# Kernel tuning notes

Measured on AMD Instinct MI355X. Metric: run time of the kernel, lower is better.

Reference implementation:

```python
import jax, jax.numpy as jnp
import numpy as np

SUBDIVISIONS = 3  # init_kwargs
EPS = 1e-6


def setup_inputs() -> dict:
    key = jax.random.key(0)
    k1, k2, k3 = jax.random.split(key, 3)
    V, K, F = 100000, 32, 64
    features = jax.random.normal(k1, (V, F), dtype=jnp.float32)
    distsq = jax.random.uniform(k2, (V, K), dtype=jnp.float32)
    neighbour_indices = jax.random.randint(k3, (V, K), 0, V, dtype=jnp.int32)
    length_scale = jnp.float32(1.0)  # non-trainable Variable, init 1.0
    return {"features": features, "distsq": distsq,
            "neighbour_indices": neighbour_indices, "length_scale": length_scale}


def reference(features, distsq, neighbour_indices, length_scale):
    # Inference path: no length-scale EMA update (training=None -> in_train_phase takes the
    # unchanged value), distsq is stop-gradient.
    distsq = jax.lax.stop_gradient(distsq)
    scaler = 10.0 * length_scale * float(SUBDIVISIONS)
    d = jnp.sqrt(distsq + EPS)                      # (V, K) neighbor distances
    nfeat = features[neighbour_indices]             # (V, K, F) gathered neighbor features
    outs = []
    for i in range(SUBDIVISIONS):
        offset = float(i) / length_scale            # radius-bin center
        w = jnp.exp(-scaler * (d - offset) ** 2)    # (V, K) Gaussian radius-bin weights
        num = jnp.einsum('vk,vkf->vf', w, nfeat)    # weighted sum over neighbors
        den = jnp.sum(w, axis=1, keepdims=True) + EPS
        outs.append(num / den)                      # soft-pixel weighted mean
    return jnp.concatenate(outs, axis=1)            # (V, SUBDIVISIONS * F)
```

## Files before the change

kernel.cpp:

```cpp
#include <hip/hip_runtime.h>

#define SP_EPS 1e-6f
typedef float f32x2 __attribute__((ext_vector_type(2)));

__device__ __forceinline__ unsigned short bf16_rne(float x) {
    unsigned u = __float_as_uint(x);
    unsigned r = u + 0x7fffu + ((u >> 16) & 1u);
    return (unsigned short)(r >> 16);
}

__global__ __launch_bounds__(256) void f32_to_bf16_kernel(
    const float* __restrict__ in, unsigned short* __restrict__ outb, int n4)
{
    int i = blockIdx.x * 256 + threadIdx.x;
    if (i >= n4) return;
    const float4 v = ((const float4*)in)[i];
    ushort4 o;
    o.x = bf16_rne(v.x); o.y = bf16_rne(v.y);
    o.z = bf16_rne(v.z); o.w = bf16_rne(v.w);
    ((ushort4*)outb)[i] = o;
}

__global__ __launch_bounds__(256) void softpixel_pk_kernel(
    const unsigned short* __restrict__ fb,
    const float* __restrict__ distsq,
    const int*   __restrict__ nidx,
    const float* __restrict__ ls_ptr,
    float*       __restrict__ out,
    int V)
{
    __shared__ f32x2 w01buf[4][32];
    __shared__ f32x2 iw2buf[4][32];
    const int lane = threadIdx.x & 63;
    const int wv   = threadIdx.x >> 6;
    const int v    = blockIdx.x * 4 + wv;
    const int h    = lane >> 5;
    const int j    = lane & 31;
    const int vc   = v < V ? v : V - 1;

    const float ls     = ls_ptr[0];
    const float scaler = 30.0f * ls;
    const float inv_ls = 1.0f / ls;

    const unsigned dvoff = (unsigned)vc * 32u + (unsigned)j;
    const float dsq = distsq[dvoff];
    const int   nb  = nidx[dvoff];
    const float d   = sqrtf(dsq + SP_EPS);
    const float t1  = d - inv_ls;
    const float t2  = d - 2.0f * inv_ls;
    const float w0  = __expf(-scaler * d  * d);
    const float w1  = __expf(-scaler * t1 * t1);
    const float w2  = __expf(-scaler * t2 * t2);
    if (h == 0) {
        w01buf[wv][j] = (f32x2){w0, w1};
        iw2buf[wv][j] = (f32x2){__int_as_float(nb), w2};
    }

    float s0 = w0, s1 = w1, s2 = w2;
    #pragma unroll
    for (int st = 1; st < 32; st <<= 1) {
        s0 += __shfl_xor(s0, st, 64);
        s1 += __shfl_xor(s1, st, 64);
        s2 += __shfl_xor(s2, st, 64);
    }
    s0 += SP_EPS; s1 += SP_EPS; s2 += SP_EPS;
    __syncthreads();

    f32x2 a01_0 = {0.f, 0.f};
    f32x2 a01_1 = {0.f, 0.f};
    float a2_0 = 0.f, a2_1 = 0.f;
    const unsigned j4 = (unsigned)(j << 2);

    #pragma unroll
    for (int kk = 0; kk < 16; ++kk) {
        const f32x2 w01 = w01buf[wv][2 * kk + h];
        const f32x2 iw2 = iw2buf[wv][2 * kk + h];
        const int   ik  = __float_as_int(iw2.x);
        const unsigned boff = ((unsigned)ik << 7) + j4;
        const unsigned fp = *(const unsigned*)((const char*)fb + boff);
        const float f0 = __uint_as_float(fp << 16);
        const float f1 = __uint_as_float(fp & 0xffff0000u);
        f32x2 f01; f01.x = f0; f01.y = f1;
        asm("v_pk_fma_f32 %0, %1, %2, %0 op_sel:[0,0,0] op_sel_hi:[1,0,1]"
            : "+v"(a01_0) : "v"(w01), "v"(f01));
        asm("v_pk_fma_f32 %0, %1, %2, %0 op_sel:[0,1,0] op_sel_hi:[1,1,1]"
            : "+v"(a01_1) : "v"(w01), "v"(f01));
        a2_0 = fmaf(iw2.y, f0, a2_0);
        a2_1 = fmaf(iw2.y, f1, a2_1);
    }

    a01_0.x += __shfl_xor(a01_0.x, 32, 64);
    a01_0.y += __shfl_xor(a01_0.y, 32, 64);
    a01_1.x += __shfl_xor(a01_1.x, 32, 64);
    a01_1.y += __shfl_xor(a01_1.y, 32, 64);
    a2_0 += __shfl_xor(a2_0, 32, 64);
    a2_1 += __shfl_xor(a2_1, 32, 64);

    if (h == 0 && v < V) {
        const float r0 = __builtin_amdgcn_rcpf(s0);
        const float r1 = __builtin_amdgcn_rcpf(s1);
        const float r2 = __builtin_amdgcn_rcpf(s2);
        float* o = out + (unsigned)v * 192u + (unsigned)(j << 1);
        o[0]   = a01_0.x * r0;  o[1]   = a01_1.x * r0;
        o[64]  = a01_0.y * r1;  o[65]  = a01_1.y * r1;
        o[128] = a2_0   * r2;   o[129] = a2_1   * r2;
    }
}

__global__ __launch_bounds__(256) void softpixel_f32_kernel(
    const float* __restrict__ feat,
    const float* __restrict__ distsq,
    const int*   __restrict__ nidx,
    const float* __restrict__ ls_ptr,
    float*       __restrict__ out,
    int V)
{
    const int lane = threadIdx.x & 63;
    const int wv   = threadIdx.x >> 6;
    const int v    = blockIdx.x * 4 + wv;
    if (v >= V) return;

    const float ls     = ls_ptr[0];
    const float scaler = 30.0f * ls;
    const float inv_ls = 1.0f / ls;

    float w0 = 0.f, w1 = 0.f, w2 = 0.f;
    int nb = 0;
    if (lane < 32) {
        const float dsq = distsq[v * 32 + lane];
        nb = nidx[v * 32 + lane];
        const float d  = sqrtf(dsq + SP_EPS);
        const float t1 = d - inv_ls;
        const float t2 = d - 2.0f * inv_ls;
        w0 = __expf(-scaler * d  * d);
        w1 = __expf(-scaler * t1 * t1);
        w2 = __expf(-scaler * t2 * t2);
    }

    float a0 = 0.f, a1 = 0.f, a2 = 0.f;
    float s0 = SP_EPS, s1 = SP_EPS, s2 = SP_EPS;
    #pragma unroll
    for (int k = 0; k < 32; ++k) {
        const int   ik = __shfl(nb, k, 64);
        const float u0 = __shfl(w0, k, 64);
        const float u1 = __shfl(w1, k, 64);
        const float u2 = __shfl(w2, k, 64);
        const float f  = feat[(size_t)ik * 64 + lane];
        a0 = fmaf(u0, f, a0);
        a1 = fmaf(u1, f, a1);
        a2 = fmaf(u2, f, a2);
        s0 += u0; s1 += u1; s2 += u2;
    }
    float* o = out + (size_t)v * 192 + lane;
    o[0]   = a0 / s0;
    o[64]  = a1 / s1;
    o[128] = a2 / s2;
}

extern "C" void kernel_launch(void* const* d_in, const int* in_sizes, int n_in,
                              void* d_out, int out_size, void* d_ws, size_t ws_size,
                              hipStream_t stream) {
    const float* feat   = (const float*)d_in[0];
    const float* distsq = (const float*)d_in[1];
    const int*   nidx   = (const int*)d_in[2];
    const float* ls     = (const float*)d_in[3];

    const int V = in_sizes[1] / 32;
    const int F = in_sizes[0] / V;
    float* out = (float*)d_out;

    const size_t need = (size_t)V * F * sizeof(unsigned short);
    const int grid = (V + 3) / 4;

    if ((size_t)ws_size >= need && F == 64) {
        unsigned short* fb = (unsigned short*)d_ws;
        const int n4 = V * F / 4;
        f32_to_bf16_kernel<<<(n4 + 255) / 256, 256, 0, stream>>>(feat, fb, n4);
        softpixel_pk_kernel<<<grid, 256, 0, stream>>>(fb, distsq, nidx, ls, out, V);
    } else {
        softpixel_f32_kernel<<<grid, 256, 0, stream>>>(feat, distsq, nidx, ls, out, V);
    }
}
```

Before: 72.43 us.

## Switch feature staging to fp16 and use v_fma_mix with permlane32 reduction

Feature rows are now staged as fp16 using packed round-toward-zero conversion instead of a manual bf16 rounding. The main kernel feeds the packed halves straight into v_fma_mix_f32, which removes the unpack shifts and masks. It also merges the per-neighbour LDS data into a single float4 read and replaces the six cross-half shuffles with three v_permlane32_swap instructions plus adds, so every lane now stores one output. Features with large magnitudes could overflow fp16 range, and round-toward-zero adds a small bias.

```diff
diff --git a/kernel.cpp b/kernel.cpp
--- a/kernel.cpp
+++ b/kernel.cpp
@@ -1,27 +1,23 @@
 #include <hip/hip_runtime.h>
 
 #define SP_EPS 1e-6f
-typedef float f32x2 __attribute__((ext_vector_type(2)));
+typedef __fp16 h2 __attribute__((ext_vector_type(2)));
 
-__device__ __forceinline__ unsigned short bf16_rne(float x) {
-    unsigned u = __float_as_uint(x);
-    unsigned r = u + 0x7fffu + ((u >> 16) & 1u);
-    return (unsigned short)(r >> 16);
-}
-
-__global__ __launch_bounds__(256) void f32_to_bf16_kernel(
-    const float* __restrict__ in, unsigned short* __restrict__ outb, int n4)
+__global__ __launch_bounds__(256) void f32_to_f16_kernel(
+    const float* __restrict__ in, unsigned* __restrict__ outh, int n4)
 {
     int i = blockIdx.x * 256 + threadIdx.x;
     if (i >= n4) return;
     const float4 v = ((const float4*)in)[i];
-    ushort4 o;
-    o.x = bf16_rne(v.x); o.y = bf16_rne(v.y);
-    o.z = bf16_rne(v.z); o.w = bf16_rne(v.w);
-    ((ushort4*)outb)[i] = o;
+    h2 p0 = __builtin_amdgcn_cvt_pkrtz(v.x, v.y);
+    h2 p1 = __builtin_amdgcn_cvt_pkrtz(v.z, v.w);
+    uint2 o;
+    o.x = *(unsigned*)&p0;
+    o.y = *(unsigned*)&p1;
+    ((uint2*)outh)[i] = o;
 }
 
-__global__ __launch_bounds__(256) void softpixel_pk_kernel(
+__global__ __launch_bounds__(256) void softpixel_mix_kernel(
     const unsigned short* __restrict__ fb,
     const float* __restrict__ distsq,
     const int*   __restrict__ nidx,
@@ -29,8 +25,7 @@
     float*       __restrict__ out,
     int V)
 {
-    __shared__ f32x2 w01buf[4][32];
-    __shared__ f32x2 iw2buf[4][32];
+    __shared__ float4 qbuf[4][32];
     const int lane = threadIdx.x & 63;
     const int wv   = threadIdx.x >> 6;
     const int v    = blockIdx.x * 4 + wv;
@@ -51,9 +46,31 @@
     const float w0  = __expf(-scaler * d  * d);
     const float w1  = __expf(-scaler * t1 * t1);
     const float w2  = __expf(-scaler * t2 * t2);
-    if (h == 0) {
-        w01buf[wv][j] = (f32x2){w0, w1};
-        iw2buf[wv][j] = (f32x2){__int_as_float(nb), w2};
+    if (h == 0)
+        qbuf[wv][j] = make_float4(__int_as_float(nb), w0, w1, w2);
+    __syncthreads();
+
+    float a0l = 0.f, a0h = 0.f, a1l = 0.f, a1h = 0.f, a2l = 0.f, a2h = 0.f;
+    const unsigned j4 = (unsigned)(j << 2);
+
+    #pragma unroll
+    for (int kk = 0; kk < 16; ++kk) {
+        const float4 q = qbuf[wv][2 * kk + h];
+        const int    ik = __float_as_int(q.x);
+        const unsigned boff = ((unsigned)ik << 7) + j4;
+        const unsigned fp = *(const unsigned*)((const char*)fb + boff);
+        asm("v_fma_mix_f32 %0, %1, %2, %0 op_sel:[0,0,0] op_sel_hi:[0,1,0]"
+            : "+v"(a0l) : "v"(q.y), "v"(fp));
+        asm("v_fma_mix_f32 %0, %1, %2, %0 op_sel:[0,1,0] op_sel_hi:[0,1,0]"
+            : "+v"(a0h) : "v"(q.y), "v"(fp));
+        asm("v_fma_mix_f32 %0, %1, %2, %0 op_sel:[0,0,0] op_sel_hi:[0,1,0]"
+            : "+v"(a1l) : "v"(q.z), "v"(fp));
+        asm("v_fma_mix_f32 %0, %1, %2, %0 op_sel:[0,1,0] op_sel_hi:[0,1,0]"
+            : "+v"(a1h) : "v"(q.z), "v"(fp));
+        asm("v_fma_mix_f32 %0, %1, %2, %0 op_sel:[0,0,0] op_sel_hi:[0,1,0]"
+            : "+v"(a2l) : "v"(q.w), "v"(fp));
+        asm("v_fma_mix_f32 %0, %1, %2, %0 op_sel:[0,1,0] op_sel_hi:[0,1,0]"
+            : "+v"(a2h) : "v"(q.w), "v"(fp));
     }
 
     float s0 = w0, s1 = w1, s2 = w2;
@@ -63,47 +80,22 @@
         s1 += __shfl_xor(s1, st, 64);
         s2 += __shfl_xor(s2, st, 64);
     }
-    s0 += SP_EPS; s1 += SP_EPS; s2 += SP_EPS;
-    __syncthreads();
+    const float r0 = __builtin_amdgcn_rcpf(s0 + SP_EPS);
+    const float r1 = __builtin_amdgcn_rcpf(s1 + SP_EPS);
+    const float r2 = __builtin_amdgcn_rcpf(s2 + SP_EPS);
 
-    f32x2 a01_0 = {0.f, 0.f};
-    f32x2 a01_1 = {0.f, 0.f};
-    float a2_0 = 0.f, a2_1 = 0.f;
-    const unsigned j4 = (unsigned)(j << 2);
+    asm("v_permlane32_swap_b32 %0, %1" : "+v"(a0l), "+v"(a0h));
+    asm("v_permlane32_swap_b32 %0, %1" : "+v"(a1l), "+v"(a1h));
+    asm("v_permlane32_swap_b32 %0, %1" : "+v"(a2l), "+v"(a2h));
+    const float c0 = a0l + a0h;
+    const float c1 = a1l + a1h;
+    const float c2 = a2l + a2h;
 
-    #pragma unroll
-    for (int kk = 0; kk < 16; ++kk) {
-        const f32x2 w01 = w01buf[wv][2 * kk + h];
-        const f32x2 iw2 = iw2buf[wv][2 * kk + h];
-        const int   ik  = __float_as_int(iw2.x);
-        const unsigned boff = ((unsigned)ik << 7) + j4;
-        const unsigned fp = *(const unsigned*)((const char*)fb + boff);
-        const float f0 = __uint_as_float(fp << 16);
-        const float f1 = __uint_as_float(fp & 0xffff0000u);
-        f32x2 f01; f01.x = f0; f01.y = f1;
-        asm("v_pk_fma_f32 %0, %1, %2, %0 op_sel:[0,0,0] op_sel_hi:[1,0,1]"
-            : "+v"(a01_0) : "v"(w01), "v"(f01));
-        asm("v_pk_fma_f32 %0, %1, %2, %0 op_sel:[0,1,0] op_sel_hi:[1,1,1]"
-            : "+v"(a01_1) : "v"(w01), "v"(f01));
-        a2_0 = fmaf(iw2.y, f0, a2_0);
-        a2_1 = fmaf(iw2.y, f1, a2_1);
-    }
-
-    a01_0.x += __shfl_xor(a01_0.x, 32, 64);
-    a01_0.y += __shfl_xor(a01_0.y, 32, 64);
-    a01_1.x += __shfl_xor(a01_1.x, 32, 64);
-    a01_1.y += __shfl_xor(a01_1.y, 32, 64);
-    a2_0 += __shfl_xor(a2_0, 32, 64);
-    a2_1 += __shfl_xor(a2_1, 32, 64);
-
-    if (h == 0 && v < V) {
-        const float r0 = __builtin_amdgcn_rcpf(s0);
-        const float r1 = __builtin_amdgcn_rcpf(s1);
-        const float r2 = __builtin_amdgcn_rcpf(s2);
-        float* o = out + (unsigned)v * 192u + (unsigned)(j << 1);
-        o[0]   = a01_0.x * r0;  o[1]   = a01_1.x * r0;
-        o[64]  = a01_0.y * r1;  o[65]  = a01_1.y * r1;
-        o[128] = a2_0   * r2;   o[129] = a2_1   * r2;
+    if (v < V) {
+        float* o = out + (unsigned)v * 192u + (unsigned)((j << 1) + h);
+        o[0]   = c0 * r0;
+        o[64]  = c1 * r1;
+        o[128] = c2 * r2;
     }
 }
 
@@ -173,10 +165,11 @@
     const int grid = (V + 3) / 4;
 
     if ((size_t)ws_size >= need && F == 64) {
-        unsigned short* fb = (unsigned short*)d_ws;
+        unsigned* fh = (unsigned*)d_ws;
         const int n4 = V * F / 4;
-        f32_to_bf16_kernel<<<(n4 + 255) / 256, 256, 0, stream>>>(feat, fb, n4);
-        softpixel_pk_kernel<<<grid, 256, 0, stream>>>(fb, distsq, nidx, ls, out, V);
+        f32_to_f16_kernel<<<(n4 + 255) / 256, 256, 0, stream>>>(feat, fh, n4);
+        softpixel_mix_kernel<<<grid, 256, 0, stream>>>(
+            (const unsigned short*)fh, distsq, nidx, ls, out, V);
     } else {
         softpixel_f32_kernel<<<grid, 256, 0, stream>>>(feat, distsq, nidx, ls, out, V);
     }
```

New measurement: 73.05 us. Within noise of the previous version (+0.9%).
